# Performance work log

Measured on AMD Instinct MI355X. Metric: run time of the kernel, lower is better.

## Reference

```python
import jax, jax.numpy as jnp
import numpy as np


def setup_inputs() -> dict:
    key = jax.random.key(0)
    k1, k2, k3, k4 = jax.random.split(key, 4)
    B, Sq, Sk, d = 16, 2048, 2048, 64
    queries = jax.random.normal(k1, (B, Sq, d), dtype=jnp.float32)
    keys = jax.random.normal(k2, (B, Sk, d), dtype=jnp.float32)
    values = jax.random.normal(k3, (B, Sk, d), dtype=jnp.float32)
    # True = padded key position (masked out)
    key_padding_mask = jax.random.randint(k4, (B, Sk), 0, 2) == 1
    return {"queries": queries, "keys": keys, "values": values,
            "key_padding_mask": key_padding_mask}


def reference(queries, keys, values, key_padding_mask):
    d = queries.shape[-1]
    # scores: [B, Sq, Sk]
    scores = jnp.einsum("bqd,bkd->bqk", queries, keys) / jnp.sqrt(
        jnp.asarray(d, dtype=queries.dtype))
    # padded keys get -inf before softmax (mask broadcast over query dim)
    scores = jnp.where(key_padding_mask[:, None, :], -jnp.inf, scores)
    attention_weights = jax.nn.softmax(scores, axis=2)
    return jnp.einsum("bqk,bkd->bqd", attention_weights, values)
```

## Files before the change

kernel.cpp:

```cpp
#include <hip/hip_runtime.h>
#include <hip/hip_bf16.h>

#define NB 16
#define SQ 2048
#define SK 2048
#define DH 64

#define KBLK 1024
#define VBLK 512
#define BBLK 128

typedef __attribute__((ext_vector_type(8))) short short8;
typedef __attribute__((ext_vector_type(8))) __bf16 bf16x8;
typedef __attribute__((ext_vector_type(4))) float floatx4;
typedef __attribute__((ext_vector_type(16))) float floatx16;
typedef __attribute__((ext_vector_type(2))) unsigned uint2v;

#define GLOB const __attribute__((address_space(1))) void*
#define LDSP __attribute__((address_space(3))) void*

__device__ __forceinline__ unsigned pk2(float a, float b) {
  __hip_bfloat162 h = __float22bfloat162_rn(make_float2(a, b));
  unsigned u; __builtin_memcpy(&u, &h, 4); return u;
}
__device__ __forceinline__ floatx16 mfma32(short8 a, short8 b, floatx16 c) {
  return __builtin_amdgcn_mfma_f32_32x32x16_bf16(
      __builtin_bit_cast(bf16x8, a), __builtin_bit_cast(bf16x8, b), c, 0, 0, 0);
}

__global__ __launch_bounds__(256)
void prepass(const float* __restrict__ K, const float* __restrict__ V,
             const int* __restrict__ m, short* __restrict__ Kb,
             short* __restrict__ Vt, float* __restrict__ bias) {
  __shared__ unsigned tlw[64 * 33];
  const int blk = blockIdx.x;
  const int t = threadIdx.x;
  if (blk < KBLK) {
    size_t i8 = ((size_t)blk * 256 + t) * 8;
    floatx4 a = *(const floatx4*)(K + i8);
    floatx4 b = *(const floatx4*)(K + i8 + 4);
    union { unsigned u[4]; short8 s; } w;
    w.u[0] = pk2(a[0], a[1]); w.u[1] = pk2(a[2], a[3]);
    w.u[2] = pk2(b[0], b[1]); w.u[3] = pk2(b[2], b[3]);
    const int local = (int)(i8 & 4095);
    const int row = local >> 6, chunk = (local >> 3) & 7;
    const size_t tb = i8 & ~(size_t)4095;
    *(short8*)(Kb + tb + row * 64 + ((chunk ^ (row & 7)) << 3)) = w.s;
  } else if (blk < KBLK + VBLK) {
    const int bt = blk - KBLK;
    const int key2 = t & 31;
    const int dg = (t >> 5) * 8;
    const float* vp0 = V + ((size_t)bt * 64 + 2 * key2) * 64 + dg;
    const float* vp1 = vp0 + 64;
    floatx4 va  = *(const floatx4*)(vp0);
    floatx4 va2 = *(const floatx4*)(vp0 + 4);
    floatx4 vb  = *(const floatx4*)(vp1);
    floatx4 vb2 = *(const floatx4*)(vp1 + 4);
#pragma unroll
    for (int j = 0; j < 4; ++j) {
      tlw[(dg + j) * 33 + key2]     = pk2(va[j],  vb[j]);
      tlw[(dg + 4 + j) * 33 + key2] = pk2(va2[j], vb2[j]);
    }
    __syncthreads();
    const short* tls = (const short*)tlw;
    short* dst = Vt + (size_t)bt * 4096;
#pragma unroll
    for (int i = 0; i < 2; ++i) {
      int idx = i * 2048 + t * 8;
      int d = idx >> 6, key = idx & 63;
      int chunk = key >> 3;
      *(short8*)(dst + d * 64 + ((chunk ^ (d & 7)) << 3)) =
          *(const short8*)(tls + d * 66 + key);
    }
  } else {
    int i = (blk - KBLK - VBLK) * 256 + t;
    bias[i] = m[i] ? -1e30f : 0.0f;
  }
}

__global__ __launch_bounds__(256, 4)
void attn_main(const float* __restrict__ Q, const short* __restrict__ Kb,
               const short* __restrict__ Vt, const float* __restrict__ bias,
               float* __restrict__ Out, float* __restrict__ Op,
               float* __restrict__ lsum) {
  __shared__ __align__(16) short ks[2][4096];
  __shared__ __align__(16) short vt[2][4096];

  const int part = blockIdx.x >> 8;
  const int rest = blockIdx.x & 255;
  const int b    = rest >> 4;
  const int qt   = rest & 15;
  const int tid  = threadIdx.x;
  const int wave = tid >> 6;
  const int lane = tid & 63;
  const int n32  = lane & 31;
  const int h    = lane >> 5;
  const int sw   = n32 & 7;
  const int q0   = qt * 128 + wave * 32;
  const int kt0  = part << 4;

  const float QS = 0.125f * 1.4426950408889634f;
  short8 qf[4];
  {
    const float* qp = Q + ((size_t)b * SQ + q0 + n32) * DH + 8 * h;
#pragma unroll
    for (int c = 0; c < 4; ++c) {
      floatx4 a  = *(const floatx4*)(qp + 16 * c);
      floatx4 a2 = *(const floatx4*)(qp + 16 * c + 4);
      union { unsigned u[4]; short8 s; } w;
      w.u[0] = pk2(a[0] * QS, a[1] * QS);
      w.u[1] = pk2(a[2] * QS, a[3] * QS);
      w.u[2] = pk2(a2[0] * QS, a2[1] * QS);
      w.u[3] = pk2(a2[2] * QS, a2[3] * QS);
      qf[c] = w.s;
    }
  }

  floatx16 o0, o1;
#pragma unroll
  for (int i = 0; i < 16; ++i) { o0[i] = 0.f; o1[i] = 0.f; }
  float l_q = 0.f;

  const short* kg = Kb + (size_t)b * SK * DH;
  const short* vg = Vt + (size_t)b * 32 * 4096;
  const float* bg = bias + b * SK + 4 * h;

  const int lo0 = (wave * 2) * 512;
  const int lo1 = (wave * 2 + 1) * 512;
  const int go0 = lo0 + lane * 8;
  const int go1 = lo1 + lane * 8;

  {
    const short* kn = kg + (size_t)kt0 * 4096;
    const short* vn = vg + (size_t)kt0 * 4096;
    __builtin_amdgcn_global_load_lds((GLOB)(kn + go0), (LDSP)&ks[0][lo0], 16, 0, 0);
    __builtin_amdgcn_global_load_lds((GLOB)(kn + go1), (LDSP)&ks[0][lo1], 16, 0, 0);
    __builtin_amdgcn_global_load_lds((GLOB)(vn + go0), (LDSP)&vt[0][lo0], 16, 0, 0);
    __builtin_amdgcn_global_load_lds((GLOB)(vn + go1), (LDSP)&vt[0][lo1], 16, 0, 0);
  }
  __syncthreads();

  int p = 0;
  for (int it = 0; it < 16; ++it) {
    const int kt = kt0 + it;
    if (it + 1 < 16) {
      const short* kn = kg + (size_t)(kt + 1) * 4096;
      const short* vn = vg + (size_t)(kt + 1) * 4096;
      __builtin_amdgcn_global_load_lds((GLOB)(kn + go0), (LDSP)&ks[p ^ 1][lo0], 16, 0, 0);
      __builtin_amdgcn_global_load_lds((GLOB)(kn + go1), (LDSP)&ks[p ^ 1][lo1], 16, 0, 0);
      __builtin_amdgcn_global_load_lds((GLOB)(vn + go0), (LDSP)&vt[p ^ 1][lo0], 16, 0, 0);
      __builtin_amdgcn_global_load_lds((GLOB)(vn + go1), (LDSP)&vt[p ^ 1][lo1], 16, 0, 0);
    }

    const float* bq = bg + kt * 64;
    floatx16 s0, s1;
#pragma unroll
    for (int u = 0; u < 4; ++u) {
      floatx4 bv0 = *(const floatx4*)(bq + 8 * u);
      floatx4 bv1 = *(const floatx4*)(bq + 32 + 8 * u);
#pragma unroll
      for (int i = 0; i < 4; ++i) { s0[4 * u + i] = bv0[i]; s1[4 * u + i] = bv1[i]; }
    }
#pragma unroll
    for (int c = 0; c < 4; ++c) {
      short8 kf0 = *(short8*)(ks[p] + n32 * 64        + ((2 * c + h) ^ sw) * 8);
      short8 kf1 = *(short8*)(ks[p] + (32 + n32) * 64 + ((2 * c + h) ^ sw) * 8);
      s0 = mfma32(kf0, qf[c], s0);
      s1 = mfma32(kf1, qf[c], s1);
    }

    uint2v pka[4], pkb[4];
    float rs = 0.f;
#pragma unroll
    for (int u = 0; u < 4; ++u) {
      float p0 = __builtin_amdgcn_exp2f(s0[4 * u + 0]);
      float p1 = __builtin_amdgcn_exp2f(s0[4 * u + 1]);
      float p2 = __builtin_amdgcn_exp2f(s0[4 * u + 2]);
      float p3 = __builtin_amdgcn_exp2f(s0[4 * u + 3]);
      float r0 = __builtin_amdgcn_exp2f(s1[4 * u + 0]);
      float r1 = __builtin_amdgcn_exp2f(s1[4 * u + 1]);
      float r2 = __builtin_amdgcn_exp2f(s1[4 * u + 2]);
      float r3 = __builtin_amdgcn_exp2f(s1[4 * u + 3]);
      rs += ((p0 + p1) + (p2 + p3)) + ((r0 + r1) + (r2 + r3));
      pka[u].x = pk2(p0, p1); pka[u].y = pk2(p2, p3);
      pkb[u].x = pk2(r0, r1); pkb[u].y = pk2(r2, r3);
    }
    l_q += rs;

#pragma unroll
    for (int c = 0; c < 4; ++c) {
      uint2v blo = (c < 2) ? pka[2 * (c & 1)]     : pkb[2 * (c & 1)];
      uint2v bhi = (c < 2) ? pka[2 * (c & 1) + 1] : pkb[2 * (c & 1) + 1];
      uint2v own  = h ? bhi : blo;
      uint2v send = h ? blo : bhi;
      uint2v recv;
      recv.x = (unsigned)__shfl_xor((int)send.x, 32);
      recv.y = (unsigned)__shfl_xor((int)send.y, 32);
      uint2v lo = h ? recv : own;
      uint2v hi = h ? own : recv;
      union { unsigned u[4]; short8 s; } pf;
      pf.u[0] = lo.x; pf.u[1] = lo.y; pf.u[2] = hi.x; pf.u[3] = hi.y;
      short8 vf0 = *(short8*)(vt[p] + n32 * 64        + ((2 * c + h) ^ sw) * 8);
      short8 vf1 = *(short8*)(vt[p] + (32 + n32) * 64 + ((2 * c + h) ^ sw) * 8);
      o0 = mfma32(vf0, pf.s, o0);
      o1 = mfma32(vf1, pf.s, o1);
    }
    __syncthreads();
    p ^= 1;
  }

  l_q += __shfl_xor(l_q, 32);

  float* Od = part ? Op : Out;
  float* orow = Od + ((size_t)b * SQ + q0 + n32) * DH;
#pragma unroll
  for (int u = 0; u < 4; ++u) {
    floatx4 w0, w1;
#pragma unroll
    for (int i = 0; i < 4; ++i) { w0[i] = o0[4 * u + i]; w1[i] = o1[4 * u + i]; }
    *(floatx4*)(orow + 8 * u + 4 * h)      = w0;
    *(floatx4*)(orow + 32 + 8 * u + 4 * h) = w1;
  }
  if (lane < 32)
    lsum[(size_t)part * NB * SQ + (size_t)b * SQ + q0 + lane] = l_q;
}

__global__ __launch_bounds__(256)
void combine(const float* __restrict__ Op, const float* __restrict__ lsum,
             float* __restrict__ Out) {
  int idx = blockIdx.x * 256 + threadIdx.x;
  int q = idx >> 3;
  int dc = (idx & 7) * 8;
  float inv = 1.0f / (lsum[q] + lsum[NB * SQ + q]);
  const size_t base = (size_t)q * DH + dc;
  floatx4 a0 = *(const floatx4*)(Out + base);
  floatx4 a1 = *(const floatx4*)(Out + base + 4);
  floatx4 b0 = *(const floatx4*)(Op + base);
  floatx4 b1 = *(const floatx4*)(Op + base + 4);
  floatx4 r0 = (a0 + b0) * inv;
  floatx4 r1 = (a1 + b1) * inv;
  *(floatx4*)(Out + base)     = r0;
  *(floatx4*)(Out + base + 4) = r1;
}

extern "C" void kernel_launch(void* const* d_in, const int* in_sizes, int n_in,
                              void* d_out, int out_size, void* d_ws, size_t ws_size,
                              hipStream_t stream) {
  const float* Q = (const float*)d_in[0];
  const float* K = (const float*)d_in[1];
  const float* V = (const float*)d_in[2];
  const int* mask = (const int*)d_in[3];
  float* Out = (float*)d_out;

  char* ws = (char*)d_ws;
  short* Kb   = (short*)(ws);
  short* Vt   = (short*)(ws + 4194304);
  float* bias = (float*)(ws + 8388608);
  float* lsum = (float*)(ws + 8519680);
  float* Op   = (float*)(ws + 8781824);

  prepass  <<<KBLK + VBLK + BBLK, 256, 0, stream>>>(K, V, mask, Kb, Vt, bias);
  attn_main<<<2 * NB * (SQ / 128), 256, 0, stream>>>(Q, Kb, Vt, bias, Out, Op, lsum);
  combine  <<<NB * SQ * DH / 8 / 256, 256, 0, stream>>>(Op, lsum, Out);
}
```

Measured before the change: 119.8 us.

## Split keys four ways and permute K rows to drop P cross-lane shuffles

```diff
diff --git a/kernel.cpp b/kernel.cpp
--- a/kernel.cpp
+++ b/kernel.cpp
@@ -26,6 +26,10 @@
 __device__ __forceinline__ floatx16 mfma32(short8 a, short8 b, floatx16 c) {
   return __builtin_amdgcn_mfma_f32_32x32x16_bf16(
       __builtin_bit_cast(bf16x8, a), __builtin_bit_cast(bf16x8, b), c, 0, 0, 0);
+}
+
+__device__ __forceinline__ int swap23(int k) {
+  return (((k >> 2) ^ (k >> 3)) & 1) ? (k ^ 12) : k;
 }
 
 __global__ __launch_bounds__(256)
@@ -43,9 +47,10 @@
     w.u[0] = pk2(a[0], a[1]); w.u[1] = pk2(a[2], a[3]);
     w.u[2] = pk2(b[0], b[1]); w.u[3] = pk2(b[2], b[3]);
     const int local = (int)(i8 & 4095);
-    const int row = local >> 6, chunk = (local >> 3) & 7;
+    const int key = local >> 6, chunk = (local >> 3) & 7;
+    const int prow = swap23(key);
     const size_t tb = i8 & ~(size_t)4095;
-    *(short8*)(Kb + tb + row * 64 + ((chunk ^ (row & 7)) << 3)) = w.s;
+    *(short8*)(Kb + tb + prow * 64 + ((chunk ^ (prow & 7)) << 3)) = w.s;
   } else if (blk < KBLK + VBLK) {
     const int bt = blk - KBLK;
     const int key2 = t & 31;
@@ -97,7 +102,7 @@
   const int h    = lane >> 5;
   const int sw   = n32 & 7;
   const int q0   = qt * 128 + wave * 32;
-  const int kt0  = part << 4;
+  const int kt0  = part << 3;
 
   const float QS = 0.125f * 1.4426950408889634f;
   short8 qf[4];
@@ -123,7 +128,7 @@
 
   const short* kg = Kb + (size_t)b * SK * DH;
   const short* vg = Vt + (size_t)b * 32 * 4096;
-  const float* bg = bias + b * SK + 4 * h;
+  const float* bg = bias + b * SK + 8 * h;
 
   const int lo0 = (wave * 2) * 512;
   const int lo1 = (wave * 2 + 1) * 512;
@@ -141,9 +146,9 @@
   __syncthreads();
 
   int p = 0;
-  for (int it = 0; it < 16; ++it) {
+  for (int it = 0; it < 8; ++it) {
     const int kt = kt0 + it;
-    if (it + 1 < 16) {
+    if (it + 1 < 8) {
       const short* kn = kg + (size_t)(kt + 1) * 4096;
       const short* vn = vg + (size_t)(kt + 1) * 4096;
       __builtin_amdgcn_global_load_lds((GLOB)(kn + go0), (LDSP)&ks[p ^ 1][lo0], 16, 0, 0);
@@ -156,8 +161,9 @@
     floatx16 s0, s1;
 #pragma unroll
     for (int u = 0; u < 4; ++u) {
-      floatx4 bv0 = *(const floatx4*)(bq + 8 * u);
-      floatx4 bv1 = *(const floatx4*)(bq + 32 + 8 * u);
+      const int off = 16 * (u >> 1) + 4 * (u & 1);
+      floatx4 bv0 = *(const floatx4*)(bq + off);
+      floatx4 bv1 = *(const floatx4*)(bq + 32 + off);
 #pragma unroll
       for (int i = 0; i < 4; ++i) { s0[4 * u + i] = bv0[i]; s1[4 * u + i] = bv1[i]; }
     }
@@ -189,17 +195,10 @@
 
 #pragma unroll
     for (int c = 0; c < 4; ++c) {
-      uint2v blo = (c < 2) ? pka[2 * (c & 1)]     : pkb[2 * (c & 1)];
-      uint2v bhi = (c < 2) ? pka[2 * (c & 1) + 1] : pkb[2 * (c & 1) + 1];
-      uint2v own  = h ? bhi : blo;
-      uint2v send = h ? blo : bhi;
-      uint2v recv;
-      recv.x = (unsigned)__shfl_xor((int)send.x, 32);
-      recv.y = (unsigned)__shfl_xor((int)send.y, 32);
-      uint2v lo = h ? recv : own;
-      uint2v hi = h ? own : recv;
+      const uint2v* X = (c < 2) ? pka : pkb;
       union { unsigned u[4]; short8 s; } pf;
-      pf.u[0] = lo.x; pf.u[1] = lo.y; pf.u[2] = hi.x; pf.u[3] = hi.y;
+      pf.u[0] = X[2 * (c & 1)].x;     pf.u[1] = X[2 * (c & 1)].y;
+      pf.u[2] = X[2 * (c & 1) + 1].x; pf.u[3] = X[2 * (c & 1) + 1].y;
       short8 vf0 = *(short8*)(vt[p] + n32 * 64        + ((2 * c + h) ^ sw) * 8);
       short8 vf1 = *(short8*)(vt[p] + (32 + n32) * 64 + ((2 * c + h) ^ sw) * 8);
       o0 = mfma32(vf0, pf.s, o0);
@@ -211,7 +210,7 @@
 
   l_q += __shfl_xor(l_q, 32);
 
-  float* Od = part ? Op : Out;
+  float* Od = part ? (Op + (size_t)(part - 1) * NB * SQ * DH) : Out;
   float* orow = Od + ((size_t)b * SQ + q0 + n32) * DH;
 #pragma unroll
   for (int u = 0; u < 4; ++u) {
@@ -231,16 +230,20 @@
   int idx = blockIdx.x * 256 + threadIdx.x;
   int q = idx >> 3;
   int dc = (idx & 7) * 8;
-  float inv = 1.0f / (lsum[q] + lsum[NB * SQ + q]);
+  float inv = 1.0f / (lsum[q] + lsum[NB * SQ + q] +
+                      lsum[2 * NB * SQ + q] + lsum[3 * NB * SQ + q]);
   const size_t base = (size_t)q * DH + dc;
+  const size_t stride = (size_t)NB * SQ * DH;
   floatx4 a0 = *(const floatx4*)(Out + base);
   floatx4 a1 = *(const floatx4*)(Out + base + 4);
   floatx4 b0 = *(const floatx4*)(Op + base);
   floatx4 b1 = *(const floatx4*)(Op + base + 4);
-  floatx4 r0 = (a0 + b0) * inv;
-  floatx4 r1 = (a1 + b1) * inv;
-  *(floatx4*)(Out + base)     = r0;
-  *(floatx4*)(Out + base + 4) = r1;
+  floatx4 c0 = *(const floatx4*)(Op + stride + base);
+  floatx4 c1 = *(const floatx4*)(Op + stride + base + 4);
+  floatx4 d0 = *(const floatx4*)(Op + 2 * stride + base);
+  floatx4 d1 = *(const floatx4*)(Op + 2 * stride + base + 4);
+  *(floatx4*)(Out + base)     = (a0 + b0 + c0 + d0) * inv;
+  *(floatx4*)(Out + base + 4) = (a1 + b1 + c1 + d1) * inv;
 }
 
 extern "C" void kernel_launch(void* const* d_in, const int* in_sizes, int n_in,
@@ -257,9 +260,9 @@
   short* Vt   = (short*)(ws + 4194304);
   float* bias = (float*)(ws + 8388608);
   float* lsum = (float*)(ws + 8519680);
-  float* Op   = (float*)(ws + 8781824);
+  float* Op   = (float*)(ws + 9043968);
 
   prepass  <<<KBLK + VBLK + BBLK, 256, 0, stream>>>(K, V, mask, Kb, Vt, bias);
-  attn_main<<<2 * NB * (SQ / 128), 256, 0, stream>>>(Q, Kb, Vt, bias, Out, Op, lsum);
+  attn_main<<<4 * NB * (SQ / 128), 256, 0, stream>>>(Q, Kb, Vt, bias, Out, Op, lsum);
   combine  <<<NB * SQ * DH / 8 / 256, 256, 0, stream>>>(Op, lsum, Out);
 }
```

Result: faster. 113.0 us (-5.7%).
